# Optimization experiments

Measured on AMD Instinct MI355X. Metric: run time of the kernel, lower is better.

The kernel has to match this reference:

```python
import jax, jax.numpy as jnp
import numpy as np

B = 4
DIM = 512          # d_model
L = 4096           # n_tokens
D_STATE = 16
D_CONV = 4
EXPAND = 2
D_INNER = EXPAND * DIM          # 1024
DT_RANK = (DIM + 15) // 16      # ceil(dim/16) = 32
EPS = 1e-5


def setup_inputs() -> dict:
    key = jax.random.key(0)
    ks = jax.random.split(key, 8)
    s = 0.02
    A_log = jnp.log(jnp.tile(jnp.arange(1.0, D_STATE + 1.0, dtype=jnp.float32), (D_INNER, 1)))
    return {
        "x": jax.random.normal(ks[0], (B, DIM, L), jnp.float32),
        "ln_w": jnp.ones((DIM,), jnp.float32),
        "ln_b": jnp.zeros((DIM,), jnp.float32),
        "W_in": jax.random.normal(ks[1], (2 * D_INNER, DIM), jnp.float32) * s,
        "conv_w": jax.random.normal(ks[2], (D_INNER, 1, D_CONV), jnp.float32) * s,
        "conv_b": jnp.zeros((D_INNER,), jnp.float32),
        "W_xproj": jax.random.normal(ks[3], (DT_RANK + 2 * D_STATE, D_INNER), jnp.float32) * s,
        "W_dt": jax.random.normal(ks[4], (D_INNER, DT_RANK), jnp.float32) * s,
        "b_dt": jax.random.normal(ks[5], (D_INNER,), jnp.float32) * 0.1,
        "A_log": A_log,
        "D": jnp.ones((D_INNER,), jnp.float32),
        "W_out": jax.random.normal(ks[6], (DIM, D_INNER), jnp.float32) * s,
    }


def reference(x, ln_w, ln_b, W_in, conv_w, conv_b, W_xproj, W_dt, b_dt, A_log, D, W_out):
    Bsz = x.shape[0]
    # [B, d_model, L] -> [B, L, d_model]
    xt = jnp.swapaxes(x, 1, 2)
    # LayerNorm
    mu = jnp.mean(xt, axis=-1, keepdims=True)
    var = jnp.mean(jnp.square(xt - mu), axis=-1, keepdims=True)
    xn = (xt - mu) * jax.lax.rsqrt(var + EPS) * ln_w + ln_b
    # in_proj -> x, z branches
    xz = xn @ W_in.T                       # [B, L, 2*d_inner]
    xin, z = jnp.split(xz, 2, axis=-1)
    # causal depthwise conv1d (torch pads d_conv-1 both sides then truncates to L)
    xc = jnp.swapaxes(xin, 1, 2)           # [B, d_inner, L]
    xc = jax.lax.conv_general_dilated(
        xc, conv_w, window_strides=(1,), padding=[(D_CONV - 1, 0)],
        dimension_numbers=("NCH", "OIH", "NCH"), feature_group_count=D_INNER)
    xc = xc + conv_b[None, :, None]
    u = jax.nn.silu(jnp.swapaxes(xc, 1, 2))  # [B, L, d_inner]
    # input-dependent SSM parameters
    dbl = u @ W_xproj.T                    # [B, L, dt_rank + 2*d_state]
    dt = dbl[..., :DT_RANK]
    Bm = dbl[..., DT_RANK:DT_RANK + D_STATE]
    Cm = dbl[..., DT_RANK + D_STATE:]
    delta = jax.nn.softplus(dt @ W_dt.T + b_dt)  # [B, L, d_inner]
    A = -jnp.exp(A_log)                    # [d_inner, d_state]

    def step(h, inp):
        d_t, b_t, c_t, u_t = inp           # [B,di], [B,ds], [B,ds], [B,di]
        dA = jnp.exp(d_t[..., None] * A)   # [B, di, ds]
        h = dA * h + (d_t * u_t)[..., None] * b_t[:, None, :]
        y = jnp.einsum("bds,bs->bd", h, c_t)
        return h, y

    h0 = jnp.zeros((Bsz, D_INNER, D_STATE), x.dtype)
    xs = (jnp.swapaxes(delta, 0, 1), jnp.swapaxes(Bm, 0, 1),
          jnp.swapaxes(Cm, 0, 1), jnp.swapaxes(u, 0, 1))
    _, ys = jax.lax.scan(step, h0, xs)     # ys: [L, B, d_inner]
    y = jnp.swapaxes(ys, 0, 1) + u * D
    y = y * jax.nn.silu(z)
    out = y @ W_out.T                      # [B, L, d_model]
    return jnp.swapaxes(out, 1, 2)         # [B, d_model, L]
```

## Files before the change

kernel.cpp:

```cpp
#include <hip/hip_runtime.h>
#include <math.h>

#define Bsz 4
#define DIM 512
#define LEN 4096
#define DST 16
#define DIN 1024
#define NCH 64
#define CHL 64
#define LDP 72

typedef unsigned short ushort_t;
typedef unsigned int uint_t;
typedef __attribute__((ext_vector_type(8))) short short8;
typedef __attribute__((ext_vector_type(8))) unsigned short ushort8;
typedef __attribute__((ext_vector_type(8))) _Float16 half8;
typedef __attribute__((ext_vector_type(4))) float f32x4;

__device__ __forceinline__ float sigmoidf_(float x){ return 1.0f/(1.0f+__expf(-x)); }
__device__ __forceinline__ float bf2f(ushort_t u){ return __uint_as_float(((uint_t)u) << 16); }
__device__ __forceinline__ ushort_t f2bf(float f){
  uint_t x = __float_as_uint(f);
  uint_t r = (x + 0x7FFFu + ((x >> 16) & 1u)) >> 16;
  return (ushort_t)r;
}
__device__ __forceinline__ ushort_t f2h_bits(float f){
  _Float16 h = (_Float16)f;
  union { _Float16 h; ushort_t u; } v; v.h = h; return v.u;
}
__device__ __forceinline__ void gl2lds16(const void* g, void* l){
  __builtin_amdgcn_global_load_lds((const __attribute__((address_space(1))) void*)g,
                                   (__attribute__((address_space(3))) void*)l, 16, 0, 0);
}
#define POW_CHAIN(av, a1) \
  { float a2=a1*a1, a4=a2*a2, a8=a4*a4; \
    av[0]=a1; av[1]=a2; av[2]=a2*a1; av[3]=a4; \
    av[4]=a4*a1; av[5]=a4*a2; av[6]=a4*av[2]; av[7]=a8; \
    av[8]=a8*a1; av[9]=a8*a2; av[10]=a8*av[2]; av[11]=a8*a4; \
    av[12]=a8*av[4]; av[13]=a8*av[5]; av[14]=a8*av[6]; av[15]=a8*a8; }

__device__ __forceinline__ bool load_nA(const float* Alog, int d, float* nA){
  bool fast = true;
  #pragma unroll
  for(int s=0;s<DST;s++){
    float v = -__expf(Alog[d*DST+s]);
    float tgt = -(float)(s+1);
    if(fabsf(v - tgt) < 1e-4f*(float)(s+1)) v = tgt;
    else fast = false;
    nA[s] = v;
  }
  return fast;
}

__global__ __launch_bounds__(256) void ln_stats_k(const float* __restrict__ x,
                                                  float* __restrict__ mu, float* __restrict__ rs){
  int bid = blockIdx.x;
  int b = bid >> 6;
  int lg = bid & 63;
  int lane = threadIdx.x & 63;
  int g = threadIdx.x >> 6;
  int l = lg*64 + lane;
  const float* xb = x + (size_t)b*DIM*LEN + l;
  float s = 0.f, sq = 0.f;
  for(int d = g*128; d < g*128 + 128; ++d){
    float v = xb[(size_t)d*LEN];
    s += v; sq += v*v;
  }
  __shared__ float rsum[4][64], rsq[4][64];
  rsum[g][lane] = s; rsq[g][lane] = sq;
  __syncthreads();
  if(threadIdx.x < 64){
    float ts = 0.f, tq = 0.f;
    for(int gg=0; gg<4; ++gg){ ts += rsum[gg][lane]; tq += rsq[gg][lane]; }
    float m = ts * (1.0f/DIM);
    float var = tq * (1.0f/DIM) - m*m;
    mu[b*LEN + l] = m;
    rs[b*LEN + l] = rsqrtf(var + 1e-5f);
  }
}

__global__ __launch_bounds__(256) void wcvt_k(const float* __restrict__ Win,
    const float* __restrict__ Wout, const float* __restrict__ Wxp,
    ushort_t* __restrict__ Winb, ushort_t* __restrict__ Woutb, ushort_t* __restrict__ Wxpb){
  int i = blockIdx.x*256 + threadIdx.x;
  if(i < 1048576) Winb[i] = f2bf(Win[i]);
  else if(i < 1572864) Woutb[i-1048576] = f2bf(Wout[i-1048576]);
  else if(i < 1638400) Wxpb[i-1572864] = f2bf(Wxp[i-1572864]);
}

__global__ __launch_bounds__(256) void xnt_k(const float* __restrict__ x,
    const float* __restrict__ mu, const float* __restrict__ rs,
    const float* __restrict__ lnw, const float* __restrict__ lnb, ushort_t* __restrict__ xnT){
  __shared__ ushort_t t[64][72];
  int bid = blockIdx.x;
  int lt = bid & 63;
  int dt_ = (bid >> 6) & 7;
  int b = bid >> 9;
  int l0 = lt*64, d0 = dt_*64;
  int ll = threadIdx.x & 63;
  int dq = threadIdx.x >> 6;
  float mul_ = mu[b*LEN + l0 + ll], rsl = rs[b*LEN + l0 + ll];
  const float* xb = x + (size_t)b*DIM*LEN;
  #pragma unroll
  for(int i=0;i<16;i++){
    int d = d0 + dq*16 + i;
    float v = xb[(size_t)d*LEN + l0 + ll];
    t[ll][dq*16 + i] = f2bf((v - mul_)*rsl*lnw[d] + lnb[d]);
  }
  __syncthreads();
  int lr = threadIdx.x >> 2, seg = threadIdx.x & 3;
  ushort_t* dst = &xnT[(size_t)(b*LEN + l0 + lr)*DIM + d0 + seg*16];
  #pragma unroll
  for(int k=0;k<4;k++){
    ushort4 v = *(const ushort4*)&t[lr][seg*16 + k*4];
    *(ushort4*)&dst[k*4] = v;
  }
}

__global__ __launch_bounds__(256) void gemm1_mfma(const ushort_t* __restrict__ A,
    const ushort_t* __restrict__ Bw, _Float16* __restrict__ xin, ushort_t* __restrict__ sz){
  __shared__ __align__(16) ushort_t smem[2*128*LDP];
  ushort_t* As = smem;
  ushort_t* Bs = smem + 128*64;
  int tid = threadIdx.x;
  int wave = tid >> 6, lane = tid & 63;
  int flat = blockIdx.y * 16 + blockIdx.x;
  int orig = (flat & 7) * 256 + (flat >> 3);
  int n0 = (orig & 15) * 128;
  int m0 = (orig >> 4) * 128;
  int wm = (wave >> 1) * 64, wn = (wave & 1) * 64;
  int lm = lane & 15;
  int lk = lane >> 4;
  int sx = lm & 7;
  f32x4 zero4 = {0.f,0.f,0.f,0.f};
  f32x4 acc[4][4];
  #pragma unroll
  for(int i=0;i<4;i++)
    #pragma unroll
    for(int j=0;j<4;j++) acc[i][j] = zero4;
  for(int k0=0; k0<512; k0+=64){
    __syncthreads();
    #pragma unroll
    for(int i=0;i<4;i++){
      int c = i*256 + tid, r = c >> 3, kc = c & 7;
      int kg = kc ^ (r & 7);
      gl2lds16(&A[(size_t)(m0 + r)*512 + k0 + kg*8], &As[c*8]);
    }
    #pragma unroll
    for(int i=0;i<4;i++){
      int c = i*256 + tid, r = c >> 3, kc = c & 7;
      int kg = kc ^ (r & 7);
      gl2lds16(&Bw[(size_t)(n0 + r)*512 + k0 + kg*8], &Bs[c*8]);
    }
    __syncthreads();
    #pragma unroll
    for(int kk=0; kk<64; kk+=32){
      short8 af[4], bf[4];
      int ch = ((kk >> 3) + lk) ^ sx;
      #pragma unroll
      for(int i=0;i<4;i++){
        af[i] = *(const short8*)&As[(wm + i*16 + lm)*64 + ch*8];
        bf[i] = *(const short8*)&Bs[(wn + i*16 + lm)*64 + ch*8];
      }
      #pragma unroll
      for(int i=0;i<4;i++)
        #pragma unroll
        for(int j=0;j<4;j++)
          acc[i][j] = __builtin_amdgcn_mfma_f32_16x16x32_bf16(af[i], bf[j], acc[i][j], 0, 0, 0);
    }
  }
  __syncthreads();
  ushort_t* T = smem;
  bool is_z = (n0 >= 1024);
  #pragma unroll
  for(int i=0;i<4;i++)
    #pragma unroll
    for(int j=0;j<4;j++)
      #pragma unroll
      for(int r=0;r<4;r++){
        int ml = wm + i*16 + lk*4 + r;
        int nl = wn + j*16 + lm;
        float v = acc[i][j][r];
        T[ml*136 + nl] = is_z ? f2bf(v * sigmoidf_(v)) : f2h_bits(v);
      }
  __syncthreads();
  int rr = tid >> 4, cc = (tid & 15)*8;
  #pragma unroll
  for(int p=0;p<8;p++){
    int row = p*16 + rr;
    ushort8 v = *(const ushort8*)&T[row*136 + cc];
    if(!is_z) *(ushort8*)((ushort_t*)xin + (size_t)(m0+row)*DIN + n0 + cc) = v;
    else      *(ushort8*)&sz[(size_t)(m0+row)*DIN + (n0-1024) + cc] = v;
  }
}

__global__ __launch_bounds__(256) void conv_silu_k(const _Float16* __restrict__ xin,
    const float* __restrict__ cw, const float* __restrict__ cb, ushort_t* __restrict__ u){
  int idx = blockIdx.x*256 + threadIdx.x;
  int dg = idx & 127;
  int lc = (idx >> 7) & 511;
  int b  = idx >> 16;
  int d0 = dg*8;
  int l0 = lc*8;
  float bias[8];
  #pragma unroll
  for(int k=0;k<8;k+=4){
    float4 c4 = *(const float4*)&cb[d0+k];
    bias[k]=c4.x; bias[k+1]=c4.y; bias[k+2]=c4.z; bias[k+3]=c4.w;
  }
  float w[8][4];
  #pragma unroll
  for(int k=0;k<8;k++){
    float4 c4 = *(const float4*)&cw[(d0+k)*4];
    w[k][0]=c4.x; w[k][1]=c4.y; w[k][2]=c4.z; w[k][3]=c4.w;
  }
  const _Float16* base = xin + ((size_t)b*LEN)*DIN + d0;
  ushort_t* ub = u + ((size_t)b*LEN)*DIN + d0;
  float f0[8], f1[8], f2[8];
  if(lc > 0){
    half8 h0 = *(const half8*)&base[(size_t)(l0-3)*DIN];
    half8 h1 = *(const half8*)&base[(size_t)(l0-2)*DIN];
    half8 h2 = *(const half8*)&base[(size_t)(l0-1)*DIN];
    #pragma unroll
    for(int k=0;k<8;k++){ f0[k]=(float)h0[k]; f1[k]=(float)h1[k]; f2[k]=(float)h2[k]; }
  } else {
    #pragma unroll
    for(int k=0;k<8;k++){ f0[k]=0.f; f1[k]=0.f; f2[k]=0.f; }
  }
  #pragma unroll
  for(int t=0;t<8;t++){
    half8 xv = *(const half8*)&base[(size_t)(l0+t)*DIN];
    float f3[8];
    #pragma unroll
    for(int k=0;k<8;k++) f3[k] = (float)xv[k];
    short8 o;
    #pragma unroll
    for(int k=0;k<8;k++){
      float a = bias[k] + f0[k]*w[k][0] + f1[k]*w[k][1] + f2[k]*w[k][2] + f3[k]*w[k][3];
      float v = a * sigmoidf_(a);
      o[k] = (short)f2bf(v);
    }
    *(short8*)&ub[(size_t)(l0+t)*DIN] = o;
    #pragma unroll
    for(int k=0;k<8;k++){ f0[k]=f1[k]; f1[k]=f2[k]; f2[k]=f3[k]; }
  }
}

__global__ __launch_bounds__(256) void gemm2_mfma(const ushort_t* __restrict__ A,
    const ushort_t* __restrict__ Bw, float* __restrict__ dbl){
  __shared__ __align__(16) ushort_t As[128*64];
  __shared__ __align__(16) ushort_t Bs[64*64];
  int tid = threadIdx.x;
  int wave = tid >> 6, lane = tid & 63;
  int m0 = blockIdx.x * 128;
  int wm = (wave >> 1) * 64, wn = (wave & 1) * 32;
  int lm = lane & 15;
  int lk = lane >> 4;
  int sx = lm & 7;
  f32x4 zero4 = {0.f,0.f,0.f,0.f};
  f32x4 acc[4][2];
  #pragma unroll
  for(int i=0;i<4;i++){ acc[i][0] = zero4; acc[i][1] = zero4; }
  for(int k0=0; k0<1024; k0+=64){
    __syncthreads();
    #pragma unroll
    for(int i=0;i<4;i++){
      int c = i*256 + tid;
      int r = c >> 3, kc = c & 7;
      int kg = kc ^ (r & 7);
      gl2lds16(&A[(size_t)(m0 + r)*1024 + k0 + kg*8], &As[c*8]);
    }
    #pragma unroll
    for(int i=0;i<2;i++){
      int c = i*256 + tid;
      int r = c >> 3, kc = c & 7;
      int kg = kc ^ (r & 7);
      gl2lds16(&Bw[(size_t)r*1024 + k0 + kg*8], &Bs[c*8]);
    }
    __syncthreads();
    #pragma unroll
    for(int kk=0; kk<64; kk+=32){
      short8 af[4], bf[2];
      int ch = ((kk >> 3) + lk) ^ sx;
      #pragma unroll
      for(int i=0;i<4;i++) af[i] = *(const short8*)&As[(wm + i*16 + lm)*64 + ch*8];
      #pragma unroll
      for(int j=0;j<2;j++) bf[j] = *(const short8*)&Bs[(wn + j*16 + lm)*64 + ch*8];
      #pragma unroll
      for(int i=0;i<4;i++)
        #pragma unroll
        for(int j=0;j<2;j++)
          acc[i][j] = __builtin_amdgcn_mfma_f32_16x16x32_bf16(af[i], bf[j], acc[i][j], 0, 0, 0);
    }
  }
  #pragma unroll
  for(int i=0;i<4;i++)
    #pragma unroll
    for(int j=0;j<2;j++)
      #pragma unroll
      for(int r=0;r<4;r++){
        int m = m0 + wm + i*16 + lk*4 + r;
        int n = wn + j*16 + lm;
        dbl[(size_t)m*64 + n] = acc[i][j][r];
      }
}

__global__ __launch_bounds__(256,4) void deltag_k(const float* __restrict__ dbl,
    const float* __restrict__ Wdt, const float* __restrict__ bdt,
    _Float16* __restrict__ dF){
  __shared__ __align__(16) float dts[64*32];
  int bid = blockIdx.x;
  int d0 = (bid & 3) * 256;
  int m0 = (bid >> 2) * 64;
  int tid = threadIdx.x;
  const f32x4* src4 = (const f32x4*)(dbl + (size_t)m0*64);
  f32x4* dst4 = (f32x4*)dts;
  for(int i=tid; i<64*8; i+=256){
    int row = i >> 3, q = i & 7;
    dst4[i] = src4[row*16 + q];
  }
  int d = d0 + tid;
  float w[32];
  #pragma unroll
  for(int k=0;k<32;k+=4){
    float4 t4 = *(const float4*)&Wdt[d*32+k];
    w[k]=t4.x; w[k+1]=t4.y; w[k+2]=t4.z; w[k+3]=t4.w;
  }
  float bd = bdt[d];
  __syncthreads();
  for(int m=0;m<64;m++){
    const float* row = dts + m*32;
    float dtv = bd;
    #pragma unroll
    for(int k=0;k<32;k+=4){
      f32x4 q = *(const f32x4*)&row[k];
      dtv += q.x*w[k] + q.y*w[k+1] + q.z*w[k+2] + q.w*w[k+3];
    }
    float dv = dtv > 15.f ? dtv : __logf(1.f + __expf(dtv));
    dF[(size_t)(m0+m)*DIN + d] = (_Float16)dv;
  }
}

__global__ __launch_bounds__(256,4) void scanA_k(const ushort_t* __restrict__ u,
    const float* __restrict__ dbl, const float* __restrict__ Alog,
    const _Float16* __restrict__ dF,
    float* __restrict__ E, float* __restrict__ cum){
  __shared__ __align__(16) float dch[CHL*16];
  int bid = blockIdx.x;
  int c = bid & (NCH-1);
  int dblk = (bid >> 6) & 3;
  int b = bid >> 8;
  int d = dblk*256 + threadIdx.x;
  const f32x4* src = (const f32x4*)(dbl + ((size_t)b*LEN + c*CHL)*64);
  f32x4* dst4 = (f32x4*)dch;
  for(int i=threadIdx.x; i<CHL*4; i+=256){
    int t = i >> 2, q = i & 3;
    dst4[i] = src[t*16 + 8 + q];
  }
  float nA[DST];
  bool fast = load_nA(Alog, d, nA);
  float Es[DST];
  #pragma unroll
  for(int s=0;s<DST;s++) Es[s] = 0.f;
  float cumD = 0.f;
  __syncthreads();
  const ushort_t*  uu = u  + ((size_t)b*LEN + c*CHL)*DIN + d;
  const _Float16*  pd = dF + ((size_t)b*LEN + c*CHL)*DIN + d;
  if(fast){
    for(int t=0;t<CHL;++t){
      float dv = (float)pd[(size_t)t*DIN];
      float uv = bf2f(uu[(size_t)t*DIN]);
      float du = dv*uv;
      cumD += dv;
      float a1 = __expf(-dv);
      float av[DST];
      POW_CHAIN(av, a1);
      const f32x4* r4 = (const f32x4*)(dch + t*16);
      f32x4 B0=r4[0], B1=r4[1], B2=r4[2], B3=r4[3];
      Es[0]=av[0]*Es[0]+du*B0.x;  Es[1]=av[1]*Es[1]+du*B0.y;
      Es[2]=av[2]*Es[2]+du*B0.z;  Es[3]=av[3]*Es[3]+du*B0.w;
      Es[4]=av[4]*Es[4]+du*B1.x;  Es[5]=av[5]*Es[5]+du*B1.y;
      Es[6]=av[6]*Es[6]+du*B1.z;  Es[7]=av[7]*Es[7]+du*B1.w;
      Es[8]=av[8]*Es[8]+du*B2.x;  Es[9]=av[9]*Es[9]+du*B2.y;
      Es[10]=av[10]*Es[10]+du*B2.z; Es[11]=av[11]*Es[11]+du*B2.w;
      Es[12]=av[12]*Es[12]+du*B3.x; Es[13]=av[13]*Es[13]+du*B3.y;
      Es[14]=av[14]*Es[14]+du*B3.z; Es[15]=av[15]*Es[15]+du*B3.w;
    }
  } else {
    for(int t=0;t<CHL;++t){
      float dv = (float)pd[(size_t)t*DIN];
      float uv = bf2f(uu[(size_t)t*DIN]);
      float du = dv*uv;
      cumD += dv;
      const float* row = dch + t*16;
      #pragma unroll
      for(int s=0;s<DST;s++){
        float a = __expf(dv*nA[s]);
        Es[s] = a*Es[s] + du*row[s];
      }
    }
  }
  size_t o = (size_t)(b*NCH + c)*DST*DIN + d;
  #pragma unroll
  for(int s=0;s<DST;s++) E[o + (size_t)s*DIN] = Es[s];
  cum[(size_t)(b*NCH + c)*DIN + d] = cumD;
}

__global__ __launch_bounds__(256) void scanB_k(const float* __restrict__ cum,
    const float* __restrict__ Alog, float* __restrict__ E){
  int g = blockIdx.x*256 + threadIdx.x;
  int d = g & 1023;
  int s = (g >> 10) & 15;
  int b = g >> 14;
  float v = -__expf(Alog[d*DST + s]);
  float tgt = -(float)(s+1);
  float nA = (fabsf(v - tgt) < 1e-4f*(float)(s+1)) ? tgt : v;
  float h = 0.f;
  for(int c=0;c<NCH;c++){
    float p = __expf(cum[(size_t)(b*NCH + c)*DIN + d] * nA);
    size_t o = (size_t)((b*NCH + c)*DST + s)*DIN + d;
    float e = E[o];
    E[o] = h;
    h = p*h + e;
  }
}

__global__ __launch_bounds__(256,4) void scanC_k(ushort_t* __restrict__ u,
    const float* __restrict__ dbl, const float* __restrict__ Alog,
    const float* __restrict__ Hs, const float* __restrict__ Dp, const ushort_t* __restrict__ sz,
    const _Float16* __restrict__ dF){
  __shared__ __align__(16) float dch[CHL*32];
  int bid = blockIdx.x;
  int c = bid & (NCH-1);
  int dblk = (bid >> 6) & 3;
  int b = bid >> 8;
  int d = dblk*256 + threadIdx.x;
  const f32x4* src = (const f32x4*)(dbl + ((size_t)b*LEN + c*CHL)*64);
  f32x4* dst4 = (f32x4*)dch;
  for(int i=threadIdx.x; i<CHL*8; i+=256){
    int t = i >> 3, q = i & 7;
    dst4[i] = src[t*16 + 8 + q];
  }
  float nA[DST];
  bool fast = load_nA(Alog, d, nA);
  float h[DST];
  size_t ho = (size_t)(b*NCH + c)*DST*DIN + d;
  #pragma unroll
  for(int s=0;s<DST;s++) h[s] = Hs[ho + (size_t)s*DIN];
  float Dv = Dp[d];
  __syncthreads();
  ushort_t* uu = u + ((size_t)b*LEN + c*CHL)*DIN + d;
  const ushort_t* zz = sz + ((size_t)b*LEN + c*CHL)*DIN + d;
  const _Float16* pd = dF + ((size_t)b*LEN + c*CHL)*DIN + d;
  if(fast){
    for(int t=0;t<CHL;++t){
      float dv = (float)pd[(size_t)t*DIN];
      float uv = bf2f(uu[(size_t)t*DIN]);
      float du = dv*uv;
      float a1 = __expf(-dv);
      float av[DST];
      POW_CHAIN(av, a1);
      const f32x4* r4 = (const f32x4*)(dch + t*32);
      f32x4 B0=r4[0], B1=r4[1], B2=r4[2], B3=r4[3];
      f32x4 C0=r4[4], C1=r4[5], C2=r4[6], C3=r4[7];
      float y0, y1, y2, y3;
      h[0]=av[0]*h[0]+du*B0.x;  h[1]=av[1]*h[1]+du*B0.y;
      h[2]=av[2]*h[2]+du*B0.z;  h[3]=av[3]*h[3]+du*B0.w;
      y0 = h[0]*C0.x + h[1]*C0.y; y1 = h[2]*C0.z + h[3]*C0.w;
      h[4]=av[4]*h[4]+du*B1.x;  h[5]=av[5]*h[5]+du*B1.y;
      h[6]=av[6]*h[6]+du*B1.z;  h[7]=av[7]*h[7]+du*B1.w;
      y2 = h[4]*C1.x + h[5]*C1.y; y3 = h[6]*C1.z + h[7]*C1.w;
      h[8]=av[8]*h[8]+du*B2.x;  h[9]=av[9]*h[9]+du*B2.y;
      h[10]=av[10]*h[10]+du*B2.z; h[11]=av[11]*h[11]+du*B2.w;
      y0 += h[8]*C2.x + h[9]*C2.y; y1 += h[10]*C2.z + h[11]*C2.w;
      h[12]=av[12]*h[12]+du*B3.x; h[13]=av[13]*h[13]+du*B3.y;
      h[14]=av[14]*h[14]+du*B3.z; h[15]=av[15]*h[15]+du*B3.w;
      y2 += h[12]*C3.x + h[13]*C3.y; y3 += h[14]*C3.z + h[15]*C3.w;
      float y = (y0+y1) + (y2+y3) + uv*Dv;
      y *= bf2f(zz[(size_t)t*DIN]);
      uu[(size_t)t*DIN] = f2bf(y);
    }
  } else {
    for(int t=0;t<CHL;++t){
      float dv = (float)pd[(size_t)t*DIN];
      float uv = bf2f(uu[(size_t)t*DIN]);
      float du = dv*uv;
      const float* row = dch + t*32;
      float y = 0.f;
      #pragma unroll
      for(int s=0;s<DST;s++){
        float a = __expf(dv*nA[s]);
        h[s] = a*h[s] + du*row[s];
        y += h[s]*row[16+s];
      }
      y += uv*Dv;
      y *= bf2f(zz[(size_t)t*DIN]);
      uu[(size_t)t*DIN] = f2bf(y);
    }
  }
}

__global__ __launch_bounds__(256) void gemm4_mfma(const ushort_t* __restrict__ A,
    const ushort_t* __restrict__ Bw, float* __restrict__ out){
  __shared__ __align__(16) ushort_t smem[2*128*LDP];
  ushort_t* As = smem;
  ushort_t* Bs = smem + 128*64;
  int tid = threadIdx.x;
  int wave = tid >> 6, lane = tid & 63;
  int flat = blockIdx.y * 4 + blockIdx.x;
  int orig = (flat & 7) * 64 + (flat >> 3);
  int n0 = (orig & 3) * 128;
  int m0 = (orig >> 2) * 128;
  int wm = (wave >> 1) * 64, wn = (wave & 1) * 64;
  int lm = lane & 15;
  int lk = lane >> 4;
  int sx = lm & 7;
  f32x4 zero4 = {0.f,0.f,0.f,0.f};
  f32x4 acc[4][4];
  #pragma unroll
  for(int i=0;i<4;i++)
    #pragma unroll
    for(int j=0;j<4;j++) acc[i][j] = zero4;
  for(int k0=0; k0<1024; k0+=64){
    __syncthreads();
    #pragma unroll
    for(int i=0;i<4;i++){
      int c = i*256 + tid, r = c >> 3, kc = c & 7;
      int kg = kc ^ (r & 7);
      gl2lds16(&A[(size_t)(m0 + r)*1024 + k0 + kg*8], &As[c*8]);
    }
    #pragma unroll
    for(int i=0;i<4;i++){
      int c = i*256 + tid, r = c >> 3, kc = c & 7;
      int kg = kc ^ (r & 7);
      gl2lds16(&Bw[(size_t)(n0 + r)*1024 + k0 + kg*8], &Bs[c*8]);
    }
    __syncthreads();
    #pragma unroll
    for(int kk=0; kk<64; kk+=32){
      short8 af[4], bf[4];
      int ch = ((kk >> 3) + lk) ^ sx;
      #pragma unroll
      for(int i=0;i<4;i++){
        af[i] = *(const short8*)&As[(wm + i*16 + lm)*64 + ch*8];
        bf[i] = *(const short8*)&Bs[(wn + i*16 + lm)*64 + ch*8];
      }
      #pragma unroll
      for(int i=0;i<4;i++)
        #pragma unroll
        for(int j=0;j<4;j++)
          acc[i][j] = __builtin_amdgcn_mfma_f32_16x16x32_bf16(af[i], bf[j], acc[i][j], 0, 0, 0);
    }
  }
  float* T = (float*)smem;
  int b = m0 >> 12, l0 = m0 & 4095;
  for(int g=0; g<4; ++g){
    __syncthreads();
    if((g >> 1) == (wave & 1)){
      int jg = g & 1;
      #pragma unroll
      for(int j2=0;j2<2;j2++){
        int j = jg*2 + j2;
        #pragma unroll
        for(int i=0;i<4;i++)
          #pragma unroll
          for(int r=0;r<4;r++){
            int ml = wm + i*16 + lk*4 + r;
            int nl = wn + j*16 + lm - g*32;
            T[nl*132 + ml] = acc[i][j][r];
          }
      }
    }
    __syncthreads();
    int nl = tid >> 3, seg = tid & 7;
    float* dst = &out[((size_t)b*DIM + n0 + g*32 + nl)*LEN + l0 + seg*16];
    #pragma unroll
    for(int k=0;k<4;k++){
      float4 v = *(const float4*)&T[nl*132 + seg*16 + k*4];
      *(float4*)&dst[k*4] = v;
    }
  }
}

extern "C" void kernel_launch(void* const* d_in, const int* in_sizes, int n_in,
                              void* d_out, int out_size, void* d_ws, size_t ws_size,
                              hipStream_t stream) {
  const float* x    = (const float*)d_in[0];
  const float* lnw  = (const float*)d_in[1];
  const float* lnb  = (const float*)d_in[2];
  const float* Win  = (const float*)d_in[3];
  const float* cw   = (const float*)d_in[4];
  const float* cb   = (const float*)d_in[5];
  const float* Wxp  = (const float*)d_in[6];
  const float* Wdt  = (const float*)d_in[7];
  const float* bdt  = (const float*)d_in[8];
  const float* Alog = (const float*)d_in[9];
  const float* Dp   = (const float*)d_in[10];
  const float* Wout = (const float*)d_in[11];
  float* out = (float*)d_out;
  float* ws  = (float*)d_ws;

  float*    mu   = ws;
  float*    rs   = ws + 16384;
  _Float16* xin  = (_Float16*)(ws + 32768);
  _Float16* dF   = (_Float16*)(ws + 32768);
  float*    E    = ws + 32768 + 8388608;
  float*    cum  = ws + 32768 + 12582912;
  ushort_t* sz   = (ushort_t*)(ws + 32768 + 16777216);
  ushort_t* u    = (ushort_t*)(ws + 32768 + 16777216 + 8388608);
  ushort_t* xnT  = (ushort_t*)(ws + 32768 + 16777216 + 16777216);
  float*    dbl  = (float*)xnT;
  ushort_t* Winb = (ushort_t*)(ws + 32768 + 16777216 + 16777216 + 4194304);
  ushort_t* Woutb= Winb + 1048576;
  ushort_t* Wxpb = Woutb + 524288;

  hipLaunchKernelGGL(ln_stats_k, dim3(256),     dim3(256), 0, stream, x, mu, rs);
  hipLaunchKernelGGL(wcvt_k,     dim3(6400),    dim3(256), 0, stream, Win, Wout, Wxp, Winb, Woutb, Wxpb);
  hipLaunchKernelGGL(xnt_k,      dim3(2048),    dim3(256), 0, stream, x, mu, rs, lnw, lnb, xnT);
  hipLaunchKernelGGL(gemm1_mfma, dim3(16,128),  dim3(256), 0, stream, xnT, Winb, xin, sz);
  hipLaunchKernelGGL(conv_silu_k,dim3(1024),    dim3(256), 0, stream, xin, cw, cb, u);
  hipLaunchKernelGGL(gemm2_mfma, dim3(128),     dim3(256), 0, stream, u, Wxpb, dbl);
  hipLaunchKernelGGL(deltag_k,   dim3(1024),    dim3(256), 0, stream, dbl, Wdt, bdt, dF);
  hipLaunchKernelGGL(scanA_k,    dim3(1024),    dim3(256), 0, stream, u, dbl, Alog, dF, E, cum);
  hipLaunchKernelGGL(scanB_k,    dim3(256),     dim3(256), 0, stream, cum, Alog, E);
  hipLaunchKernelGGL(scanC_k,    dim3(1024),    dim3(256), 0, stream, u, dbl, Alog, E, Dp, sz, dF);
  hipLaunchKernelGGL(gemm4_mfma, dim3(4,128),   dim3(256), 0, stream, u, Woutb, out);
}
```

Before: 360.8 us.

## Double-buffer LDS tiles in the three MFMA GEMMs to overlap loads with compute

Converts the gemm1, gemm2 and gemm4 k-loops to a two-stage LDS ping-pong. The async global-to-LDS copy for the next k-tile is issued before the MFMAs run on the current tile, and each iteration now has one barrier instead of two. This aims to hide global load latency behind matrix math. It doubles LDS use (64 KB per block for gemm1/gemm4), which may cut occupancy. Correctness depends on the copy being complete at the single barrier.

```diff
diff --git a/kernel.cpp b/kernel.cpp
--- a/kernel.cpp
+++ b/kernel.cpp
@@ -8,7 +8,6 @@
 #define DIN 1024
 #define NCH 64
 #define CHL 64
-#define LDP 72
 
 typedef unsigned short ushort_t;
 typedef unsigned int uint_t;
@@ -119,9 +118,7 @@
 
 __global__ __launch_bounds__(256) void gemm1_mfma(const ushort_t* __restrict__ A,
     const ushort_t* __restrict__ Bw, _Float16* __restrict__ xin, ushort_t* __restrict__ sz){
-  __shared__ __align__(16) ushort_t smem[2*128*LDP];
-  ushort_t* As = smem;
-  ushort_t* Bs = smem + 128*64;
+  __shared__ __align__(16) ushort_t smem[2*16384];
   int tid = threadIdx.x;
   int wave = tid >> 6, lane = tid & 63;
   int flat = blockIdx.y * 16 + blockIdx.x;
@@ -138,21 +135,30 @@
   for(int i=0;i<4;i++)
     #pragma unroll
     for(int j=0;j<4;j++) acc[i][j] = zero4;
-  for(int k0=0; k0<512; k0+=64){
-    __syncthreads();
-    #pragma unroll
-    for(int i=0;i<4;i++){
-      int c = i*256 + tid, r = c >> 3, kc = c & 7;
-      int kg = kc ^ (r & 7);
-      gl2lds16(&A[(size_t)(m0 + r)*512 + k0 + kg*8], &As[c*8]);
-    }
-    #pragma unroll
-    for(int i=0;i<4;i++){
-      int c = i*256 + tid, r = c >> 3, kc = c & 7;
-      int kg = kc ^ (r & 7);
-      gl2lds16(&Bw[(size_t)(n0 + r)*512 + k0 + kg*8], &Bs[c*8]);
-    }
-    __syncthreads();
+  #pragma unroll
+  for(int i=0;i<4;i++){
+    int c = i*256 + tid, r = c >> 3, kc = c & 7;
+    int kg = kc ^ (r & 7);
+    gl2lds16(&A [(size_t)(m0 + r)*512 + kg*8], &smem[c*8]);
+    gl2lds16(&Bw[(size_t)(n0 + r)*512 + kg*8], &smem[8192 + c*8]);
+  }
+  __syncthreads();
+  int cur = 0;
+  for(int t=0; t<8; ++t){
+    if(t < 7){
+      int k0n = (t+1)*64;
+      ushort_t* Ad = &smem[(cur^1)*16384];
+      ushort_t* Bd = &smem[(cur^1)*16384 + 8192];
+      #pragma unroll
+      for(int i=0;i<4;i++){
+        int c = i*256 + tid, r = c >> 3, kc = c & 7;
+        int kg = kc ^ (r & 7);
+        gl2lds16(&A [(size_t)(m0 + r)*512 + k0n + kg*8], &Ad[c*8]);
+        gl2lds16(&Bw[(size_t)(n0 + r)*512 + k0n + kg*8], &Bd[c*8]);
+      }
+    }
+    const ushort_t* As = &smem[cur*16384];
+    const ushort_t* Bs = &smem[cur*16384 + 8192];
     #pragma unroll
     for(int kk=0; kk<64; kk+=32){
       short8 af[4], bf[4];
@@ -168,8 +174,9 @@
         for(int j=0;j<4;j++)
           acc[i][j] = __builtin_amdgcn_mfma_f32_16x16x32_bf16(af[i], bf[j], acc[i][j], 0, 0, 0);
     }
-  }
-  __syncthreads();
+    __syncthreads();
+    cur ^= 1;
+  }
   ushort_t* T = smem;
   bool is_z = (n0 >= 1024);
   #pragma unroll
@@ -248,8 +255,7 @@
 
 __global__ __launch_bounds__(256) void gemm2_mfma(const ushort_t* __restrict__ A,
     const ushort_t* __restrict__ Bw, float* __restrict__ dbl){
-  __shared__ __align__(16) ushort_t As[128*64];
-  __shared__ __align__(16) ushort_t Bs[64*64];
+  __shared__ __align__(16) ushort_t smem[2*12288];
   int tid = threadIdx.x;
   int wave = tid >> 6, lane = tid & 63;
   int m0 = blockIdx.x * 128;
@@ -261,23 +267,40 @@
   f32x4 acc[4][2];
   #pragma unroll
   for(int i=0;i<4;i++){ acc[i][0] = zero4; acc[i][1] = zero4; }
-  for(int k0=0; k0<1024; k0+=64){
-    __syncthreads();
-    #pragma unroll
-    for(int i=0;i<4;i++){
-      int c = i*256 + tid;
-      int r = c >> 3, kc = c & 7;
-      int kg = kc ^ (r & 7);
-      gl2lds16(&A[(size_t)(m0 + r)*1024 + k0 + kg*8], &As[c*8]);
-    }
-    #pragma unroll
-    for(int i=0;i<2;i++){
-      int c = i*256 + tid;
-      int r = c >> 3, kc = c & 7;
-      int kg = kc ^ (r & 7);
-      gl2lds16(&Bw[(size_t)r*1024 + k0 + kg*8], &Bs[c*8]);
-    }
-    __syncthreads();
+  #pragma unroll
+  for(int i=0;i<4;i++){
+    int c = i*256 + tid, r = c >> 3, kc = c & 7;
+    int kg = kc ^ (r & 7);
+    gl2lds16(&A[(size_t)(m0 + r)*1024 + kg*8], &smem[c*8]);
+  }
+  #pragma unroll
+  for(int i=0;i<2;i++){
+    int c = i*256 + tid, r = c >> 3, kc = c & 7;
+    int kg = kc ^ (r & 7);
+    gl2lds16(&Bw[(size_t)r*1024 + kg*8], &smem[8192 + c*8]);
+  }
+  __syncthreads();
+  int cur = 0;
+  for(int t=0; t<16; ++t){
+    if(t < 15){
+      int k0n = (t+1)*64;
+      ushort_t* Ad = &smem[(cur^1)*12288];
+      ushort_t* Bd = &smem[(cur^1)*12288 + 8192];
+      #pragma unroll
+      for(int i=0;i<4;i++){
+        int c = i*256 + tid, r = c >> 3, kc = c & 7;
+        int kg = kc ^ (r & 7);
+        gl2lds16(&A[(size_t)(m0 + r)*1024 + k0n + kg*8], &Ad[c*8]);
+      }
+      #pragma unroll
+      for(int i=0;i<2;i++){
+        int c = i*256 + tid, r = c >> 3, kc = c & 7;
+        int kg = kc ^ (r & 7);
+        gl2lds16(&Bw[(size_t)r*1024 + k0n + kg*8], &Bd[c*8]);
+      }
+    }
+    const ushort_t* As = &smem[cur*12288];
+    const ushort_t* Bs = &smem[cur*12288 + 8192];
     #pragma unroll
     for(int kk=0; kk<64; kk+=32){
       short8 af[4], bf[2];
@@ -292,6 +315,8 @@
         for(int j=0;j<2;j++)
           acc[i][j] = __builtin_amdgcn_mfma_f32_16x16x32_bf16(af[i], bf[j], acc[i][j], 0, 0, 0);
     }
+    __syncthreads();
+    cur ^= 1;
   }
   #pragma unroll
   for(int i=0;i<4;i++)
@@ -502,9 +527,7 @@
 
 __global__ __launch_bounds__(256) void gemm4_mfma(const ushort_t* __restrict__ A,
     const ushort_t* __restrict__ Bw, float* __restrict__ out){
-  __shared__ __align__(16) ushort_t smem[2*128*LDP];
-  ushort_t* As = smem;
-  ushort_t* Bs = smem + 128*64;
+  __shared__ __align__(16) ushort_t smem[2*16384];
   int tid = threadIdx.x;
   int wave = tid >> 6, lane = tid & 63;
   int flat = blockIdx.y * 4 + blockIdx.x;
@@ -521,21 +544,30 @@
   for(int i=0;i<4;i++)
     #pragma unroll
     for(int j=0;j<4;j++) acc[i][j] = zero4;
-  for(int k0=0; k0<1024; k0+=64){
-    __syncthreads();
-    #pragma unroll
-    for(int i=0;i<4;i++){
-      int c = i*256 + tid, r = c >> 3, kc = c & 7;
-      int kg = kc ^ (r & 7);
-      gl2lds16(&A[(size_t)(m0 + r)*1024 + k0 + kg*8], &As[c*8]);
-    }
-    #pragma unroll
-    for(int i=0;i<4;i++){
-      int c = i*256 + tid, r = c >> 3, kc = c & 7;
-      int kg = kc ^ (r & 7);
-      gl2lds16(&Bw[(size_t)(n0 + r)*1024 + k0 + kg*8], &Bs[c*8]);
-    }
-    __syncthreads();
+  #pragma unroll
+  for(int i=0;i<4;i++){
+    int c = i*256 + tid, r = c >> 3, kc = c & 7;
+    int kg = kc ^ (r & 7);
+    gl2lds16(&A [(size_t)(m0 + r)*1024 + kg*8], &smem[c*8]);
+    gl2lds16(&Bw[(size_t)(n0 + r)*1024 + kg*8], &smem[8192 + c*8]);
+  }
+  __syncthreads();
+  int cur = 0;
+  for(int t=0; t<16; ++t){
+    if(t < 15){
+      int k0n = (t+1)*64;
+      ushort_t* Ad = &smem[(cur^1)*16384];
+      ushort_t* Bd = &smem[(cur^1)*16384 + 8192];
+      #pragma unroll
+      for(int i=0;i<4;i++){
+        int c = i*256 + tid, r = c >> 3, kc = c & 7;
+        int kg = kc ^ (r & 7);
+        gl2lds16(&A [(size_t)(m0 + r)*1024 + k0n + kg*8], &Ad[c*8]);
+        gl2lds16(&Bw[(size_t)(n0 + r)*1024 + k0n + kg*8], &Bd[c*8]);
+      }
+    }
+    const ushort_t* As = &smem[cur*16384];
+    const ushort_t* Bs = &smem[cur*16384 + 8192];
     #pragma unroll
     for(int kk=0; kk<64; kk+=32){
       short8 af[4], bf[4];
@@ -551,6 +583,8 @@
         for(int j=0;j<4;j++)
           acc[i][j] = __builtin_amdgcn_mfma_f32_16x16x32_bf16(af[i], bf[j], acc[i][j], 0, 0, 0);
     }
+    __syncthreads();
+    cur ^= 1;
   }
   float* T = (float*)smem;
   int b = m0 >> 12, l0 = m0 & 4095;
```

New measurement: 350.4 us. 2.9% less time.
